# Optimization experiments

Hardware: AMD Instinct MI355X
Metric: run time of the kernel (lower is better)

The kernel has to match this reference:

```python
import jax, jax.numpy as jnp
import numpy as np

N, E, D, H, L = 50000, 800000, 256, 256, 40
HIDLAYERS = 3
NEG_SLOPE = 0.2  # PyG GATConv default leaky_relu slope


def _add_self_loops(edge_index, n):
    loop = jnp.arange(n, dtype=edge_index.dtype)
    src = jnp.concatenate([edge_index[0], loop])
    dst = jnp.concatenate([edge_index[1], loop])
    return src, dst


def gcn_conv(x, edge_index, W, b, n):
    # PyG GCNConv: add self-loops, symmetric deg^-1/2 normalization, linear, scatter-add
    src, dst = _add_self_loops(edge_index, n)
    ones = jnp.ones(src.shape[0], dtype=x.dtype)
    deg = jax.ops.segment_sum(ones, dst, num_segments=n)
    dinv = jnp.where(deg > 0, jax.lax.rsqrt(deg), 0.0)
    h = x @ W  # [n, out]
    norm = dinv[src] * dinv[dst]  # [E+n]
    out = jax.ops.segment_sum(h[src] * norm[:, None], dst, num_segments=n)
    return out + b


def gat_conv(x, edge_index, W, a_src, a_dst, b, n):
    # PyG GATConv (heads=1): add self-loops, e = leaky_relu(a_src.h_j + a_dst.h_i),
    # softmax over incoming edges per destination node, weighted scatter-add
    src, dst = _add_self_loops(edge_index, n)
    h = x @ W  # [n, H]
    al_src = h @ a_src  # [n]
    al_dst = h @ a_dst  # [n]
    e = jax.nn.leaky_relu(al_src[src] + al_dst[dst], NEG_SLOPE)  # [E+n]
    # numerically stable segment softmax over dst (self-loops => no empty segments)
    m = jax.ops.segment_max(e, dst, num_segments=n)
    ex = jnp.exp(e - m[dst])
    z = jax.ops.segment_sum(ex, dst, num_segments=n)
    alpha = ex / z[dst]
    out = jax.ops.segment_sum(h[src] * alpha[:, None], dst, num_segments=n)
    return out + b


def setup_inputs() -> dict:
    key = jax.random.key(0)
    ks = jax.random.split(key, 8)
    s = 0.05
    return {
        "x": jax.random.normal(ks[0], (N, D), jnp.float32),
        "edge_index": jax.random.randint(ks[1], (2, E), 0, N, dtype=jnp.int64),
        "W1": jax.random.normal(ks[2], (D, H), jnp.float32) * s,
        "b1": jnp.zeros((H,), jnp.float32),
        "Wg": jax.random.normal(ks[3], (H, H), jnp.float32) * s,
        "a_src": jax.random.normal(ks[4], (H,), jnp.float32) * s,
        "a_dst": jax.random.normal(ks[5], (H,), jnp.float32) * s,
        "bg": jnp.zeros((H,), jnp.float32),
        "W2": jax.random.normal(ks[6], (H, L), jnp.float32) * s,
        "b2": jnp.zeros((L,), jnp.float32),
    }


def reference(x, edge_index, W1, b1, Wg, a_src, a_dst, bg, W2, b2):
    n = x.shape[0]
    # feature standardization (torch .std is unbiased, ddof=1)
    x = (x - x.mean(axis=0, keepdims=True)) / x.std(axis=0, keepdims=True, ddof=1)
    x = jax.nn.relu(gcn_conv(x, edge_index, W1, b1, n))  # dropout = identity (eval)
    for _ in range(HIDLAYERS - 1):
        x = jax.nn.relu(gat_conv(x, edge_index, Wg, a_src, a_dst, bg, n))
    x = gcn_conv(x, edge_index, W2, b2, n)
    return jax.nn.log_softmax(x, axis=1)
```

## Files before the change

kernel.cpp:

```cpp
#include <hip/hip_runtime.h>
#include <math.h>

#define DD 256
#define LL 40
#define NSLOPE 0.2f

typedef unsigned short u16;
typedef unsigned int uint;
typedef __attribute__((ext_vector_type(8))) short short8;
typedef __attribute__((ext_vector_type(4))) float f32x4;

__device__ __forceinline__ float bf2f(u16 v) { return __uint_as_float(((uint)v) << 16); }
__device__ __forceinline__ u16 f2bf(float f) {
  uint u = __float_as_uint(f);
  return (u16)((u + 0x7fff + ((u >> 16) & 1)) >> 16);
}
__device__ __forceinline__ void acc8(float* a, uint4 v) {
  a[0] += __uint_as_float(v.x << 16);
  a[1] += __uint_as_float(v.x & 0xffff0000u);
  a[2] += __uint_as_float(v.y << 16);
  a[3] += __uint_as_float(v.y & 0xffff0000u);
  a[4] += __uint_as_float(v.z << 16);
  a[5] += __uint_as_float(v.z & 0xffff0000u);
  a[6] += __uint_as_float(v.w << 16);
  a[7] += __uint_as_float(v.w & 0xffff0000u);
}
__device__ __forceinline__ void wacc8(float* a, uint4 v, float w) {
  a[0] += w * __uint_as_float(v.x << 16);
  a[1] += w * __uint_as_float(v.x & 0xffff0000u);
  a[2] += w * __uint_as_float(v.y << 16);
  a[3] += w * __uint_as_float(v.y & 0xffff0000u);
  a[4] += w * __uint_as_float(v.z << 16);
  a[5] += w * __uint_as_float(v.z & 0xffff0000u);
  a[6] += w * __uint_as_float(v.w << 16);
  a[7] += w * __uint_as_float(v.w & 0xffff0000u);
}

__global__ void k_colstats(const float* __restrict__ x, float* __restrict__ csum,
                           float* __restrict__ csq, int n, int rowsPerBlk) {
  int col = threadIdx.x;
  int r0 = blockIdx.x * rowsPerBlk;
  int r1 = min(r0 + rowsPerBlk, n);
  float s = 0.f, q = 0.f;
  for (int r = r0; r < r1; ++r) {
    float v = x[(size_t)r * DD + col];
    s += v; q += v * v;
  }
  atomicAdd(&csum[col], s);
  atomicAdd(&csq[col], q);
}

__global__ void k_finalize_stats(const float* __restrict__ csum, const float* __restrict__ csq,
                                 float* __restrict__ mean, float* __restrict__ rstd, int n) {
  int j = threadIdx.x;
  float s = csum[j], q = csq[j];
  float m = s / (float)n;
  float var = (q - s * m) / (float)(n - 1);
  mean[j] = m;
  rstd[j] = 1.0f / sqrtf(var);
}

__global__ void k_standardize(const float* __restrict__ x, const float* __restrict__ mean,
                              const float* __restrict__ rstd, u16* __restrict__ xs, int total4) {
  int i = blockIdx.x * blockDim.x + threadIdx.x;
  if (i >= total4) return;
  int c4 = i & (DD / 4 - 1);
  float4 v = ((const float4*)x)[i];
  float4 m = ((const float4*)mean)[c4];
  float4 r = ((const float4*)rstd)[c4];
  uint2 o;
  o.x = (uint)f2bf((v.x - m.x) * r.x) | ((uint)f2bf((v.y - m.y) * r.y) << 16);
  o.y = (uint)f2bf((v.z - m.z) * r.z) | ((uint)f2bf((v.w - m.w) * r.w) << 16);
  ((uint2*)xs)[i] = o;
}

__global__ void k_convWt(const float* __restrict__ W, u16* __restrict__ Wt, int K, int N) {
  int k = blockIdx.x;
  for (int nn = threadIdx.x; nn < N; nn += blockDim.x)
    Wt[(size_t)nn * K + k] = f2bf(W[(size_t)k * N + nn]);
}

__global__ void k_count_deg(const int* __restrict__ edst, int E, int* __restrict__ degi) {
  int i = blockIdx.x * blockDim.x + threadIdx.x;
  if (i < E) atomicAdd(&degi[edst[i]], 1);
}

__global__ __launch_bounds__(1024) void k_scan(const int* __restrict__ degi,
                                               int* __restrict__ rowptr, int n) {
  const int T = 1024;
  __shared__ int sums[T];
  int tid = threadIdx.x;
  int per = (n + T - 1) / T;
  int a = tid * per;
  int b = min(a + per, n);
  int local = 0;
  for (int i = a; i < b; ++i) local += degi[i] + 1;
  sums[tid] = local;
  __syncthreads();
  for (int off = 1; off < T; off <<= 1) {
    int v = 0;
    if (tid >= off) v = sums[tid - off];
    __syncthreads();
    if (tid >= off) sums[tid] += v;
    __syncthreads();
  }
  int run = (tid > 0) ? sums[tid - 1] : 0;
  for (int i = a; i < b; ++i) { rowptr[i] = run; run += degi[i] + 1; }
  if (tid == T - 1) rowptr[n] = run;
}

__global__ void k_prep_nodes(const int* __restrict__ degi, const int* __restrict__ rowptr,
                             float* __restrict__ dinv, int* __restrict__ cursor, int n) {
  int i = blockIdx.x * blockDim.x + threadIdx.x;
  if (i < n) {
    dinv[i] = 1.0f / sqrtf((float)(degi[i] + 1));
    cursor[i] = rowptr[i];
  }
}

__global__ void k_scatter(const int* __restrict__ esrc, const int* __restrict__ edst, int E,
                          int* __restrict__ cursor, int* __restrict__ csrsrc) {
  int i = blockIdx.x * blockDim.x + threadIdx.x;
  if (i < E) {
    int d = edst[i];
    int p = atomicAdd(&cursor[d], 1);
    csrsrc[p] = esrc[i];
  }
}

__global__ void k_selfloop(const int* __restrict__ rowptr, int* __restrict__ csrsrc, int n) {
  int i = blockIdx.x * blockDim.x + threadIdx.x;
  if (i < n) csrsrc[rowptr[i + 1] - 1] = i;
}

__global__ __launch_bounds__(256) void k_mfma_gemm(const u16* __restrict__ A, const u16* __restrict__ Bt,
                                                   u16* __restrict__ C, int M, int N, int K,
                                                   const float* __restrict__ rowScale) {
  __shared__ u16 As[128 * 40];
  __shared__ u16 Bs[64 * 40];
  int tid = threadIdx.x;
  int wave = tid >> 6, lane = tid & 63, quad = lane >> 4, l16 = lane & 15;
  int rowBase = blockIdx.y * 128, colBase = blockIdx.x * 64;
  f32x4 acc[2][4] = {};
  for (int k0 = 0; k0 < K; k0 += 32) {
    #pragma unroll
    for (int i = 0; i < 2; ++i) {
      int ch = tid + i * 256;
      int r = ch >> 2, cc = (ch & 3) * 8;
      int gr = rowBase + r;
      uint4 v = make_uint4(0, 0, 0, 0);
      if (gr < M) v = *(const uint4*)(A + (size_t)gr * K + k0 + cc);
      *(uint4*)&As[r * 40 + cc] = v;
    }
    {
      int r = tid >> 2, cc = (tid & 3) * 8;
      int gn = colBase + r;
      uint4 v = make_uint4(0, 0, 0, 0);
      if (gn < N) v = *(const uint4*)(Bt + (size_t)gn * K + k0 + cc);
      *(uint4*)&Bs[r * 40 + cc] = v;
    }
    __syncthreads();
    short8 af[2];
    af[0] = *(const short8*)&As[(wave * 32 + l16) * 40 + quad * 8];
    af[1] = *(const short8*)&As[(wave * 32 + 16 + l16) * 40 + quad * 8];
    short8 bf[4];
    #pragma unroll
    for (int j = 0; j < 4; ++j) bf[j] = *(const short8*)&Bs[(j * 16 + l16) * 40 + quad * 8];
    #pragma unroll
    for (int i = 0; i < 2; ++i)
      #pragma unroll
      for (int j = 0; j < 4; ++j)
        acc[i][j] = __builtin_amdgcn_mfma_f32_16x16x32_bf16(af[i], bf[j], acc[i][j], 0, 0, 0);
    __syncthreads();
  }
  #pragma unroll
  for (int i = 0; i < 2; ++i) {
    #pragma unroll
    for (int r = 0; r < 4; ++r) {
      int gr = rowBase + wave * 32 + i * 16 + quad * 4 + r;
      if (gr >= M) continue;
      float sc = rowScale ? rowScale[gr] : 1.0f;
      #pragma unroll
      for (int j = 0; j < 4; ++j) {
        int gc = colBase + j * 16 + l16;
        if (gc < N) C[(size_t)gr * N + gc] = f2bf(acc[i][j][r] * sc);
      }
    }
  }
}

__global__ __launch_bounds__(256) void k_gcn_agg(const u16* __restrict__ hs, const int* __restrict__ rowptr,
                                                 const int* __restrict__ csrsrc, const float* __restrict__ dinv,
                                                 const float* __restrict__ bias, u16* __restrict__ out, int n) {
  int wave = (blockIdx.x * blockDim.x + threadIdx.x) >> 6;
  int lane = threadIdx.x & 63;
  int sub = lane >> 5, l = lane & 31;
  int w = wave * 2 + sub;
  if (w >= n) return;
  int p0 = rowptr[w], p1 = rowptr[w + 1];
  float a[8] = {};
  int p = p0;
  for (; p + 4 <= p1; p += 4) {
    int s0 = csrsrc[p], s1 = csrsrc[p + 1], s2 = csrsrc[p + 2], s3 = csrsrc[p + 3];
    uint4 v0 = *(const uint4*)(hs + (size_t)s0 * DD + l * 8);
    uint4 v1 = *(const uint4*)(hs + (size_t)s1 * DD + l * 8);
    uint4 v2 = *(const uint4*)(hs + (size_t)s2 * DD + l * 8);
    uint4 v3 = *(const uint4*)(hs + (size_t)s3 * DD + l * 8);
    acc8(a, v0); acc8(a, v1); acc8(a, v2); acc8(a, v3);
  }
  for (; p < p1; ++p) {
    int s = csrsrc[p];
    uint4 v = *(const uint4*)(hs + (size_t)s * DD + l * 8);
    acc8(a, v);
  }
  float dd = dinv[w];
  float4 b0 = ((const float4*)bias)[l * 2];
  float4 b1 = ((const float4*)bias)[l * 2 + 1];
  float r0 = fmaxf(dd * a[0] + b0.x, 0.f), r1 = fmaxf(dd * a[1] + b0.y, 0.f);
  float r2 = fmaxf(dd * a[2] + b0.z, 0.f), r3 = fmaxf(dd * a[3] + b0.w, 0.f);
  float r4 = fmaxf(dd * a[4] + b1.x, 0.f), r5 = fmaxf(dd * a[5] + b1.y, 0.f);
  float r6 = fmaxf(dd * a[6] + b1.z, 0.f), r7 = fmaxf(dd * a[7] + b1.w, 0.f);
  uint4 o;
  o.x = (uint)f2bf(r0) | ((uint)f2bf(r1) << 16);
  o.y = (uint)f2bf(r2) | ((uint)f2bf(r3) << 16);
  o.z = (uint)f2bf(r4) | ((uint)f2bf(r5) << 16);
  o.w = (uint)f2bf(r6) | ((uint)f2bf(r7) << 16);
  *(uint4*)(out + (size_t)w * DD + l * 8) = o;
}

__global__ __launch_bounds__(256) void k_al(const u16* __restrict__ h, const float* __restrict__ va,
                                            const float* __restrict__ vb, float* __restrict__ als,
                                            float* __restrict__ ald, int n) {
  int w = (blockIdx.x * blockDim.x + threadIdx.x) >> 6;
  int lane = threadIdx.x & 63;
  if (w >= n) return;
  uint2 v = *(const uint2*)(h + (size_t)w * DD + lane * 4);
  float x0 = __uint_as_float(v.x << 16), x1 = __uint_as_float(v.x & 0xffff0000u);
  float x2 = __uint_as_float(v.y << 16), x3 = __uint_as_float(v.y & 0xffff0000u);
  float4 a = ((const float4*)va)[lane];
  float4 b = ((const float4*)vb)[lane];
  float s1 = x0 * a.x + x1 * a.y + x2 * a.z + x3 * a.w;
  float s2 = x0 * b.x + x1 * b.y + x2 * b.z + x3 * b.w;
  #pragma unroll
  for (int off = 1; off < 64; off <<= 1) {
    s1 += __shfl_xor(s1, off);
    s2 += __shfl_xor(s2, off);
  }
  if (lane == 0) { als[w] = s1; ald[w] = s2; }
}

__global__ __launch_bounds__(256) void k_gat_agg(const u16* __restrict__ h, const int* __restrict__ rowptr,
                                                 const int* __restrict__ csrsrc, const float* __restrict__ als,
                                                 const float* __restrict__ ald, const float* __restrict__ bias,
                                                 u16* __restrict__ out, int n) {
  int wave = (blockIdx.x * blockDim.x + threadIdx.x) >> 6;
  int lane = threadIdx.x & 63;
  int sub = lane >> 5, l = lane & 31;
  int w = wave * 2 + sub;
  if (w >= n) return;
  float ad = ald[w];
  int p0 = rowptr[w], p1 = rowptr[w + 1];
  float m = -1e30f, z = 0.f;
  for (int p = p0 + l; p < p1; p += 32) {
    float e = als[csrsrc[p]] + ad;
    e = (e > 0.f) ? e : NSLOPE * e;
    if (e > m) { z = z * __expf(m - e) + 1.f; m = e; }
    else z += __expf(e - m);
  }
  #pragma unroll
  for (int off = 16; off >= 1; off >>= 1) {
    float m2 = __shfl_xor(m, off), z2 = __shfl_xor(z, off);
    float M = fmaxf(m, m2);
    z = z * __expf(m - M) + z2 * __expf(m2 - M);
    m = M;
  }
  float invz = 1.0f / z;
  float a[8] = {};
  int p = p0;
  for (; p + 4 <= p1; p += 4) {
    int s0 = csrsrc[p], s1 = csrsrc[p + 1], s2 = csrsrc[p + 2], s3 = csrsrc[p + 3];
    float e0 = als[s0] + ad; e0 = (e0 > 0.f) ? e0 : NSLOPE * e0;
    float e1 = als[s1] + ad; e1 = (e1 > 0.f) ? e1 : NSLOPE * e1;
    float e2 = als[s2] + ad; e2 = (e2 > 0.f) ? e2 : NSLOPE * e2;
    float e3 = als[s3] + ad; e3 = (e3 > 0.f) ? e3 : NSLOPE * e3;
    uint4 v0 = *(const uint4*)(h + (size_t)s0 * DD + l * 8);
    uint4 v1 = *(const uint4*)(h + (size_t)s1 * DD + l * 8);
    uint4 v2 = *(const uint4*)(h + (size_t)s2 * DD + l * 8);
    uint4 v3 = *(const uint4*)(h + (size_t)s3 * DD + l * 8);
    wacc8(a, v0, __expf(e0 - m) * invz);
    wacc8(a, v1, __expf(e1 - m) * invz);
    wacc8(a, v2, __expf(e2 - m) * invz);
    wacc8(a, v3, __expf(e3 - m) * invz);
  }
  for (; p < p1; ++p) {
    int s = csrsrc[p];
    float e = als[s] + ad; e = (e > 0.f) ? e : NSLOPE * e;
    uint4 v = *(const uint4*)(h + (size_t)s * DD + l * 8);
    wacc8(a, v, __expf(e - m) * invz);
  }
  float4 b0 = ((const float4*)bias)[l * 2];
  float4 b1 = ((const float4*)bias)[l * 2 + 1];
  float r0 = fmaxf(a[0] + b0.x, 0.f), r1 = fmaxf(a[1] + b0.y, 0.f);
  float r2 = fmaxf(a[2] + b0.z, 0.f), r3 = fmaxf(a[3] + b0.w, 0.f);
  float r4 = fmaxf(a[4] + b1.x, 0.f), r5 = fmaxf(a[5] + b1.y, 0.f);
  float r6 = fmaxf(a[6] + b1.z, 0.f), r7 = fmaxf(a[7] + b1.w, 0.f);
  uint4 o;
  o.x = (uint)f2bf(r0) | ((uint)f2bf(r1) << 16);
  o.y = (uint)f2bf(r2) | ((uint)f2bf(r3) << 16);
  o.z = (uint)f2bf(r4) | ((uint)f2bf(r5) << 16);
  o.w = (uint)f2bf(r6) | ((uint)f2bf(r7) << 16);
  *(uint4*)(out + (size_t)w * DD + l * 8) = o;
}

__global__ __launch_bounds__(256) void k_gcn2_lsm(const u16* __restrict__ hs, const int* __restrict__ rowptr,
                                                  const int* __restrict__ csrsrc, const float* __restrict__ dinv,
                                                  const float* __restrict__ bias, float* __restrict__ out, int n) {
  int w = (blockIdx.x * blockDim.x + threadIdx.x) >> 6;
  int lane = threadIdx.x & 63;
  if (w >= n) return;
  int p0 = rowptr[w], p1 = rowptr[w + 1];
  float acc = 0.f;
  int p = p0;
  for (; p + 4 <= p1; p += 4) {
    int s0 = csrsrc[p], s1 = csrsrc[p + 1], s2 = csrsrc[p + 2], s3 = csrsrc[p + 3];
    if (lane < LL) {
      float v0 = bf2f(hs[(size_t)s0 * LL + lane]);
      float v1 = bf2f(hs[(size_t)s1 * LL + lane]);
      float v2 = bf2f(hs[(size_t)s2 * LL + lane]);
      float v3 = bf2f(hs[(size_t)s3 * LL + lane]);
      acc += v0 + v1 + v2 + v3;
    }
  }
  for (; p < p1; ++p) {
    int s = csrsrc[p];
    if (lane < LL) acc += bf2f(hs[(size_t)s * LL + lane]);
  }
  float dd = dinv[w];
  float v = (lane < LL) ? dd * acc + bias[lane] : -INFINITY;
  float m = v;
  #pragma unroll
  for (int off = 1; off < 64; off <<= 1) m = fmaxf(m, __shfl_xor(m, off));
  float ex = (lane < LL) ? __expf(v - m) : 0.f;
  float z = ex;
  #pragma unroll
  for (int off = 1; off < 64; off <<= 1) z += __shfl_xor(z, off);
  if (lane < LL) out[(size_t)w * LL + lane] = v - m - logf(z);
}

extern "C" void kernel_launch(void* const* d_in, const int* in_sizes, int n_in,
                              void* d_out, int out_size, void* d_ws, size_t ws_size,
                              hipStream_t stream) {
  const float* x   = (const float*)d_in[0];
  const int*   ei  = (const int*)d_in[1];
  const float* W1  = (const float*)d_in[2];
  const float* b1  = (const float*)d_in[3];
  const float* Wg  = (const float*)d_in[4];
  const float* a_s = (const float*)d_in[5];
  const float* a_d = (const float*)d_in[6];
  const float* bg  = (const float*)d_in[7];
  const float* W2  = (const float*)d_in[8];
  const float* b2  = (const float*)d_in[9];
  float* out = (float*)d_out;

  const int n = in_sizes[0] / DD;
  const int E = in_sizes[1] / 2;
  const int M = E + n;
  const int* esrc = ei;
  const int* edst = ei + E;

  char* wp = (char*)d_ws;
  auto carve = [&](size_t bytes) -> char* {
    char* p = wp;
    wp += (bytes + 255) & ~(size_t)255;
    return p;
  };
  u16*   buf0   = (u16*)carve((size_t)n * DD * 2);
  u16*   buf1   = (u16*)carve((size_t)n * DD * 2);
  u16*   h40    = (u16*)carve((size_t)n * LL * 2);
  u16*   W1t    = (u16*)carve((size_t)DD * DD * 2);
  u16*   Wgt    = (u16*)carve((size_t)DD * DD * 2);
  u16*   W2t    = (u16*)carve((size_t)LL * DD * 2);
  int*   csrsrc = (int*)carve((size_t)M * 4);
  int*   rowptr = (int*)carve((size_t)(n + 1) * 4);
  int*   cursor = (int*)carve((size_t)n * 4);
  int*   degi   = (int*)carve((size_t)n * 4);
  float* dinv   = (float*)carve((size_t)n * 4);
  float* als    = (float*)carve((size_t)n * 4);
  float* ald    = (float*)carve((size_t)n * 4);
  float* csum   = (float*)carve(DD * 4);
  float* csq    = (float*)carve(DD * 4);
  float* mean   = (float*)carve(DD * 4);
  float* rstd   = (float*)carve(DD * 4);

  hipMemsetAsync(degi, 0, (size_t)n * 4, stream);
  hipMemsetAsync(csum, 0, DD * 4, stream);
  hipMemsetAsync(csq, 0, DD * 4, stream);

  const int rowsPerBlk = 128;
  k_colstats<<<(n + rowsPerBlk - 1) / rowsPerBlk, DD, 0, stream>>>(x, csum, csq, n, rowsPerBlk);
  k_finalize_stats<<<1, DD, 0, stream>>>(csum, csq, mean, rstd, n);
  int total4 = n * (DD / 4);
  k_standardize<<<(total4 + 255) / 256, 256, 0, stream>>>(x, mean, rstd, buf0, total4);

  k_convWt<<<DD, 256, 0, stream>>>(W1, W1t, DD, DD);
  k_convWt<<<DD, 256, 0, stream>>>(Wg, Wgt, DD, DD);
  k_convWt<<<DD, 64, 0, stream>>>(W2, W2t, DD, LL);

  k_count_deg<<<(E + 255) / 256, 256, 0, stream>>>(edst, E, degi);
  k_scan<<<1, 1024, 0, stream>>>(degi, rowptr, n);
  k_prep_nodes<<<(n + 255) / 256, 256, 0, stream>>>(degi, rowptr, dinv, cursor, n);
  k_scatter<<<(E + 255) / 256, 256, 0, stream>>>(esrc, edst, E, cursor, csrsrc);
  k_selfloop<<<(n + 255) / 256, 256, 0, stream>>>(rowptr, csrsrc, n);

  dim3 blk(256);
  dim3 gemmGrid((DD + 63) / 64, (n + 127) / 128);
  int aggGrid1 = (n + 3) / 4;
  int aggGrid2 = (n + 7) / 8;

  k_mfma_gemm<<<gemmGrid, blk, 0, stream>>>(buf0, W1t, buf1, n, DD, DD, dinv);
  k_gcn_agg<<<aggGrid2, blk, 0, stream>>>(buf1, rowptr, csrsrc, dinv, b1, buf0, n);

  for (int l = 0; l < 2; ++l) {
    k_mfma_gemm<<<gemmGrid, blk, 0, stream>>>(buf0, Wgt, buf1, n, DD, DD, nullptr);
    k_al<<<aggGrid1, blk, 0, stream>>>(buf1, a_s, a_d, als, ald, n);
    k_gat_agg<<<aggGrid2, blk, 0, stream>>>(buf1, rowptr, csrsrc, als, ald, bg, buf0, n);
  }

  dim3 gemmGrid2(1, (n + 127) / 128);
  k_mfma_gemm<<<gemmGrid2, blk, 0, stream>>>(buf0, W2t, h40, n, LL, DD, dinv);
  k_gcn2_lsm<<<aggGrid1, blk, 0, stream>>>(h40, rowptr, csrsrc, dinv, b2, out, n);
}
```

Baseline: 667.1 us.

## Replace single-block degree scan with multi-block scan fused with node prep

Replaces the single 1024-thread block prefix scan over node degrees with a three-kernel scan: per-chunk block sums, a one-wavefront scan of those sums, and a parallel rowptr write. The final stage also writes cursor and dinv, so the separate node-prep kernel is removed. The aim is to stop serialising the scan on one compute unit, where each thread walked about fifty strided elements. It adds one kernel launch, and the block-sum scan assumes at most 64 chunks, which holds for n=50000.

```diff
diff --git a/kernel.cpp b/kernel.cpp
--- a/kernel.cpp
+++ b/kernel.cpp
@@ -4,6 +4,7 @@
 #define DD 256
 #define LL 40
 #define NSLOPE 0.2f
+#define SCHUNK 1024
 
 typedef unsigned short u16;
 typedef unsigned int uint;
@@ -85,36 +86,66 @@
   if (i < E) atomicAdd(&degi[edst[i]], 1);
 }
 
-__global__ __launch_bounds__(1024) void k_scan(const int* __restrict__ degi,
-                                               int* __restrict__ rowptr, int n) {
-  const int T = 1024;
-  __shared__ int sums[T];
-  int tid = threadIdx.x;
-  int per = (n + T - 1) / T;
-  int a = tid * per;
-  int b = min(a + per, n);
-  int local = 0;
-  for (int i = a; i < b; ++i) local += degi[i] + 1;
-  sums[tid] = local;
+__global__ __launch_bounds__(256) void k_blocksum(const int* __restrict__ degi, int* __restrict__ bsum, int n) {
+  int b = blockIdx.x, tid = threadIdx.x;
+  int base = b * SCHUNK;
+  int end = min(base + SCHUNK, n);
+  int s = 0;
+  for (int i = base + tid; i < end; i += 256) s += degi[i] + 1;
+  __shared__ int ws[4];
+  #pragma unroll
+  for (int off = 32; off >= 1; off >>= 1) s += __shfl_down(s, off);
+  if ((tid & 63) == 0) ws[tid >> 6] = s;
   __syncthreads();
-  for (int off = 1; off < T; off <<= 1) {
+  if (tid == 0) bsum[b] = ws[0] + ws[1] + ws[2] + ws[3];
+}
+
+__global__ void k_scan_bsums(int* __restrict__ bsum, int nb) {
+  int lane = threadIdx.x;
+  int orig = (lane < nb) ? bsum[lane] : 0;
+  int v = orig;
+  #pragma unroll
+  for (int off = 1; off < 64; off <<= 1) {
+    int t = __shfl_up(v, off);
+    if (lane >= off) v += t;
+  }
+  if (lane < nb) bsum[lane] = v - orig;
+}
+
+__global__ __launch_bounds__(256) void k_rowptr_write(const int* __restrict__ degi, const int* __restrict__ bsum,
+                                                      int* __restrict__ rowptr, int* __restrict__ cursor,
+                                                      float* __restrict__ dinv, int n) {
+  int b = blockIdx.x, tid = threadIdx.x;
+  int base = b * SCHUNK + tid * 4;
+  int d[4];
+  int t = 0;
+  #pragma unroll
+  for (int j = 0; j < 4; ++j) {
+    int i = base + j;
+    d[j] = (i < n) ? degi[i] + 1 : 0;
+    t += d[j];
+  }
+  __shared__ int sc[256];
+  sc[tid] = t;
+  __syncthreads();
+  for (int off = 1; off < 256; off <<= 1) {
     int v = 0;
-    if (tid >= off) v = sums[tid - off];
+    if (tid >= off) v = sc[tid - off];
     __syncthreads();
-    if (tid >= off) sums[tid] += v;
+    if (tid >= off) sc[tid] += v;
     __syncthreads();
   }
-  int run = (tid > 0) ? sums[tid - 1] : 0;
-  for (int i = a; i < b; ++i) { rowptr[i] = run; run += degi[i] + 1; }
-  if (tid == T - 1) rowptr[n] = run;
-}
-
-__global__ void k_prep_nodes(const int* __restrict__ degi, const int* __restrict__ rowptr,
-                             float* __restrict__ dinv, int* __restrict__ cursor, int n) {
-  int i = blockIdx.x * blockDim.x + threadIdx.x;
-  if (i < n) {
-    dinv[i] = 1.0f / sqrtf((float)(degi[i] + 1));
-    cursor[i] = rowptr[i];
+  int run = bsum[b] + sc[tid] - t;
+  #pragma unroll
+  for (int j = 0; j < 4; ++j) {
+    int i = base + j;
+    if (i < n) {
+      rowptr[i] = run;
+      cursor[i] = run;
+      dinv[i] = rsqrtf((float)d[j]);
+      run += d[j];
+      if (i == n - 1) rowptr[n] = run;
+    }
   }
 }
 
@@ -384,6 +415,7 @@
   int*   rowptr = (int*)carve((size_t)(n + 1) * 4);
   int*   cursor = (int*)carve((size_t)n * 4);
   int*   degi   = (int*)carve((size_t)n * 4);
+  int*   bsum   = (int*)carve(64 * 4);
   float* dinv   = (float*)carve((size_t)n * 4);
   float* als    = (float*)carve((size_t)n * 4);
   float* ald    = (float*)carve((size_t)n * 4);
@@ -406,9 +438,11 @@
   k_convWt<<<DD, 256, 0, stream>>>(Wg, Wgt, DD, DD);
   k_convWt<<<DD, 64, 0, stream>>>(W2, W2t, DD, LL);
 
+  int nb = (n + SCHUNK - 1) / SCHUNK;
   k_count_deg<<<(E + 255) / 256, 256, 0, stream>>>(edst, E, degi);
-  k_scan<<<1, 1024, 0, stream>>>(degi, rowptr, n);
-  k_prep_nodes<<<(n + 255) / 256, 256, 0, stream>>>(degi, rowptr, dinv, cursor, n);
+  k_blocksum<<<nb, 256, 0, stream>>>(degi, bsum, n);
+  k_scan_bsums<<<1, 64, 0, stream>>>(bsum, nb);
+  k_rowptr_write<<<nb, 256, 0, stream>>>(degi, bsum, rowptr, cursor, dinv, n);
   k_scatter<<<(E + 255) / 256, 256, 0, stream>>>(esrc, edst, E, cursor, csrsrc);
   k_selfloop<<<(n + 255) / 256, 256, 0, stream>>>(rowptr, csrsrc, n);
 
```

Measured after the change: 598.1 us. -10.3%, faster.
